# Kernel optimization log

Measured on AMD Instinct MI355X. Metric: run time of the kernel, lower is better.

## Reference

```python
import jax, jax.numpy as jnp
import numpy as np

B, T, ADIM = 64, 2048, 384
NUM_EMB, HID_DIM = 10, 3


def setup_inputs() -> dict:
    key = jax.random.key(0)
    ks = jax.random.split(key, 9)
    return {
        "hs_ref_embs": jax.random.normal(ks[0], (B, T, ADIM), dtype=jnp.float32),
        "inds": jax.random.randint(ks[1], (B, T), 0, NUM_EMB, dtype=jnp.int64),
        "codebook": jax.random.normal(ks[2], (NUM_EMB, HID_DIM), dtype=jnp.float32),
        "W_ih": jax.random.normal(ks[3], (4 * NUM_EMB, ADIM), dtype=jnp.float32) * 0.05,
        "W_hh": jax.random.normal(ks[4], (4 * NUM_EMB, NUM_EMB), dtype=jnp.float32) * 0.05,
        "b_ih": jax.random.normal(ks[5], (4 * NUM_EMB,), dtype=jnp.float32) * 0.05,
        "b_hh": jax.random.normal(ks[6], (4 * NUM_EMB,), dtype=jnp.float32) * 0.05,
        "qs_W": jax.random.normal(ks[7], (ADIM, HID_DIM), dtype=jnp.float32) * 0.05,
        "qs_b": jax.random.normal(ks[8], (ADIM,), dtype=jnp.float32) * 0.05,
    }


def _lstm_cell(x, h, c, W_ih, W_hh, b_ih, b_hh):
    # PyTorch LSTMCell: gates = x @ W_ih^T + b_ih + h @ W_hh^T + b_hh
    gates = x @ W_ih.T + b_ih + h @ W_hh.T + b_hh  # (B, 4H)
    i, f, g, o = jnp.split(gates, 4, axis=-1)
    i, f, o = jax.nn.sigmoid(i), jax.nn.sigmoid(f), jax.nn.sigmoid(o)
    g = jnp.tanh(g)
    c_new = f * c + i * g
    h_new = o * jnp.tanh(c_new)
    return h_new, c_new


def reference(hs_ref_embs, inds, codebook, W_ih, W_hh, b_ih, b_hh, qs_W, qs_b):
    Bsz, Tmax, _ = hs_ref_embs.shape
    H = codebook.shape[0]  # num_embeddings (= LSTM hidden size)
    D = codebook.shape[1]  # hidden_dim

    def step(carry, xs):
        h, c, prev_emb = carry
        x_t, is_first = xs
        qs = prev_emb @ qs_W.T + qs_b  # (B, adim)
        inp = jnp.where(is_first, x_t, x_t + qs)
        h, c = _lstm_cell(inp, h, c, W_ih, W_hh, b_ih, b_hh)
        scores = jax.nn.log_softmax(h, axis=-1)  # (B, H)
        top_ind = jnp.argmax(scores, axis=-1)    # top-1, indices not differentiated
        emb = codebook[top_ind]                  # (B, D) gather == one-hot matmul
        return (h, c, emb), (scores, emb)

    init = (
        jnp.zeros((Bsz, H), hs_ref_embs.dtype),
        jnp.zeros((Bsz, H), hs_ref_embs.dtype),
        jnp.zeros((Bsz, D), hs_ref_embs.dtype),
    )
    xs = (jnp.swapaxes(hs_ref_embs, 0, 1), jnp.arange(Tmax) == 0)
    _, (scores, embs) = jax.lax.scan(step, init, xs)
    scores = jnp.swapaxes(scores, 0, 1)  # (B, T, H) log-probs
    embs = jnp.swapaxes(embs, 0, 1)      # (B, T, D)
    # NLLLoss(mean): -mean over (B,T) of log-prob at ground-truth index
    picked = jnp.take_along_axis(scores, inds[..., None], axis=-1)[..., 0]
    loss = -jnp.mean(picked)
    return embs, loss
```

## Files before the change

kernel.cpp:

```cpp
#include <hip/hip_runtime.h>
#include <math.h>

#define BB 64
#define TT 2048
#define ADIM 384
#define NE 10
#define NG 40
#define HD 3

#define OFF_X64   0ULL
#define OFF_W64T  41943040ULL
#define OFF_ETAB  (OFF_W64T + 122880ULL)
#define OFF_ADD0  (OFF_ETAB + 3200ULL)
#define OFF_ADD1  (OFF_ADD0 + 320ULL)
#define OFF_H     (OFF_ADD1 + 320ULL)
#define OFF_IDX   (OFF_H + 5242880ULL)
#define OFF_PART  (OFF_IDX + 524288ULL)
#define OFF_DUMP  (OFF_PART + 4096ULL)

__device__ __forceinline__ float fexp2(float x) {
    float r;
    asm("v_exp_f32 %0, %1" : "=v"(r) : "v"(x));
    return r;
}
__device__ __forceinline__ float frcp1(float d) {
    float r;
    asm("v_rcp_f32 %0, %1" : "=v"(r) : "v"(d));
    float e = fmaf(-d, r, 1.0f);
    return fmaf(r, e, r);
}

template<int CTRL>
__device__ __forceinline__ float dpp_mov_f32(float x) {
    int v = __float_as_int(x);
    v = __builtin_amdgcn_update_dpp(v, v, CTRL, 0xF, 0xF, true);
    return __int_as_float(v);
}
template<int CTRL, int RMASK>
__device__ __forceinline__ unsigned dpp_mov_u32(unsigned x) {
    int v = __builtin_amdgcn_update_dpp((int)x, (int)x, CTRL, RMASK, 0xF, true);
    return (unsigned)v;
}
__device__ __forceinline__ unsigned umax2(unsigned a, unsigned b) {
    return a > b ? a : b;
}

__global__ __launch_bounds__(256) void setup_kernel(
        const float* __restrict__ W_ih, const float* __restrict__ codebook,
        const float* __restrict__ qs_W, const float* __restrict__ qs_b,
        const float* __restrict__ b_ih, const float* __restrict__ b_hh,
        double* __restrict__ W64T, float* __restrict__ Etab32,
        double* __restrict__ ADD0, double* __restrict__ ADD1) {
    int tid = threadIdx.x;
    if (blockIdx.x == 0) {
        if (tid < NG) {
            int k = tid;
            double M0 = 0, M1 = 0, M2 = 0, qb = 0;
            for (int a = 0; a < ADIM; ++a) {
                double w = (double)W_ih[k * ADIM + a];
                M0 = fma(w, (double)qs_W[a * HD + 0], M0);
                M1 = fma(w, (double)qs_W[a * HD + 1], M1);
                M2 = fma(w, (double)qs_W[a * HD + 2], M2);
                qb = fma(w, (double)qs_b[a], qb);
            }
            for (int i = 0; i < NE; ++i) {
                double e = (double)codebook[i * HD + 0] * M0;
                e = fma((double)codebook[i * HD + 1], M1, e);
                e = fma((double)codebook[i * HD + 2], M2, e);
                Etab32[i * NG + k] = (float)e;
            }
            double bias = (double)b_ih[k] + (double)b_hh[k];
            ADD0[k] = bias;
            ADD1[k] = bias + qb;
        }
    } else {
        int i = (blockIdx.x - 1) * 256 + tid;
        int a = i / NG, kk = i % NG;
        W64T[i] = (double)W_ih[kk * ADIM + a];
    }
}

__global__ __launch_bounds__(256) void gemm_kernel(
        const float* __restrict__ hs, const double* __restrict__ W64T,
        const double* __restrict__ ADD0, const double* __restrict__ ADD1,
        float* __restrict__ X32) {
    int lane = threadIdx.x & 63;
    int wv = threadIdx.x >> 6;
    int cb = __builtin_amdgcn_readfirstlane(wv * 10);
    long row = (long)blockIdx.x * 64 + lane;
    const float* xr = hs + row * ADIM;
    double acc[10];
#pragma unroll
    for (int j = 0; j < 10; ++j) acc[j] = 0.0;
    for (int a0 = 0; a0 < ADIM; a0 += 4) {
        float4 xv = *(const float4*)(xr + a0);
#pragma unroll
        for (int u = 0; u < 4; ++u) {
            double xd = (double)((&xv.x)[u]);
            const double* wp = W64T + (a0 + u) * NG + cb;
#pragma unroll
            for (int j = 0; j < 10; ++j) acc[j] = fma(wp[j], xd, acc[j]);
        }
    }
    int trow = (int)(row & (TT - 1));
    float* op = X32 + row * NG + cb;
#pragma unroll
    for (int j = 0; j < 10; ++j) {
        double a0j = ADD0[cb + j], a1j = ADD1[cb + j];
        op[j] = (float)(acc[j] + (trow == 0 ? a0j : a1j));
    }
}

__global__ __launch_bounds__(64) void recur_kernel(
        const float* __restrict__ X32,
        const float* __restrict__ W_hh, const float* __restrict__ Etab32,
        char* __restrict__ ws) {
    const int k = threadIdx.x;
    const int b = blockIdx.x;
    const int j = k & 3;
    const int m = k >> 2;
    const bool valid = (k < NG);
    const int col = valid ? (j * 10 + m) : (NG - 1);
    const bool isg = (j == 2);

    const float LOG2E = 1.44269504088896340736f;
    const float Lg   = isg ? (-2.0f * LOG2E) : (-LOG2E);
    const float amul = isg ? 2.0f : 1.0f;
    const float aadd = isg ? -1.0f : 0.0f;
    const float L2   = -2.0f * LOG2E;

    float whh[NE];
#pragma unroll
    for (int mm = 0; mm < NE; ++mm) whh[mm] = W_hh[col * NE + mm];
    float etab[NE];
#pragma unroll
    for (int i = 0; i < NE; ++i) etab[i] = Etab32[i * NG + col];

    const float* Xb = X32 + (long)b * TT * NG;

    const bool is_h = ((k & 3) == 0) && valid;
    const bool is_i = (k == NG);
    unsigned voff = is_h ? (unsigned)(OFF_H + ((unsigned)b * TT * NE + m) * 4u)
                  : is_i ? (unsigned)(OFF_IDX + (unsigned)b * TT * 4u)
                         : (unsigned)OFF_DUMP;
    const unsigned vstep = is_h ? (unsigned)(NE * 4) : is_i ? 4u : 0u;

    const unsigned vmask = valid ? 0xFFFFFFFFu : 0u;

    float xs0 = Xb[0 * NG + col];
    float xs1 = Xb[1 * NG + col];
    float xs2 = Xb[2 * NG + col];
    float xs3 = Xb[3 * NG + col];

    float ha[NE];
#pragma unroll
    for (int mm = 0; mm < NE; ++mm) ha[mm] = 0.0f;
    float c = 0.0f, esel = 0.0f;

    auto step = [&](float& xslot, int t) {
        float xg = xslot;
        xslot = Xb[(t + 4) * NG + col];

        float p0 = fmaf(ha[1], whh[1], ha[0] * whh[0]);
        float p1 = fmaf(ha[3], whh[3], ha[2] * whh[2]);
        float p2 = fmaf(ha[5], whh[5], ha[4] * whh[4]);
        float p3 = fmaf(ha[7], whh[7], ha[6] * whh[6]);
        float p4 = fmaf(ha[9], whh[9], ha[8] * whh[8]);
        float dotE = ((p0 + p1) + (p2 + p3)) + (p4 + esel);
        float g32 = xg + dotE;

        float e1 = fexp2(g32 * Lg);
        float r1 = frcp1(1.0f + e1);
        float act = fmaf(amul, r1, aadd);

        float fiv = dpp_mov_f32<0x00>(act);
        float ffv = dpp_mov_f32<0x55>(act);
        float fgv = dpp_mov_f32<0xAA>(act);
        float fov = dpp_mov_f32<0xFF>(act);
        c = fmaf(ffv, c, fiv * fgv);

        float e2 = fexp2(fabsf(c) * L2);
        float r2 = frcp1(1.0f + e2);
        float th = fmaf(2.0f, r2, -1.0f);
        float habs = fov * th;
        int hI = __float_as_int(habs) | (__float_as_int(c) & 0x80000000);

        int smsk = hI >> 31;
        unsigned key0 = ((unsigned)(hI ^ (smsk | (int)0x80000000))) & vmask;
        unsigned kr = umax2(key0, dpp_mov_u32<0x124, 0xF>(key0));
        kr = umax2(kr, dpp_mov_u32<0x128, 0xF>(kr));
        kr = umax2(kr, dpp_mov_u32<0x142, 0xA>(kr));
        kr = umax2(kr, dpp_mov_u32<0x143, 0xC>(kr));
        unsigned sMax = (unsigned)__builtin_amdgcn_readlane((int)kr, 32);
        unsigned long long ball = __ballot(key0 == sMax);
        int s_idx = ((int)__builtin_ctzll(ball)) >> 2;

        int val = is_h ? hI : s_idx;
        *(int*)(ws + voff) = val;
        voff += vstep;

#pragma unroll
        for (int mm = 0; mm < NE; ++mm)
            ha[mm] = __int_as_float(__builtin_amdgcn_readlane(hI, 4 * mm));

        float a0 = (s_idx & 1) ? etab[1] : etab[0];
        float a1 = (s_idx & 1) ? etab[3] : etab[2];
        float a2 = (s_idx & 1) ? etab[5] : etab[4];
        float a3 = (s_idx & 1) ? etab[7] : etab[6];
        float a4 = (s_idx & 1) ? etab[9] : etab[8];
        float b0 = (s_idx & 2) ? a1 : a0;
        float b1 = (s_idx & 2) ? a3 : a2;
        float c0 = (s_idx & 4) ? b1 : b0;
        esel = (s_idx & 8) ? a4 : c0;
    };

    for (int t = 0; t < TT; t += 4) {
        step(xs0, t);
        step(xs1, t + 1);
        step(xs2, t + 2);
        step(xs3, t + 3);
    }
}

__global__ __launch_bounds__(256) void tail_kernel(
        const float* __restrict__ h_ws, const int* __restrict__ idx_ws,
        const int* __restrict__ inds, const float* __restrict__ codebook,
        float* __restrict__ out_embs, double* __restrict__ partials) {
    int i = blockIdx.x * 256 + threadIdx.x;
    int idx = idx_ws[i];
    out_embs[i * 3 + 0] = codebook[idx * 3 + 0];
    out_embs[i * 3 + 1] = codebook[idx * 3 + 1];
    out_embs[i * 3 + 2] = codebook[idx * 3 + 2];

    const float* hp = h_ws + (long)i * NE;
    double hv[NE];
#pragma unroll
    for (int mm = 0; mm < NE; ++mm) hv[mm] = (double)hp[mm];
    double mx = hv[0];
#pragma unroll
    for (int mm = 1; mm < NE; ++mm) mx = fmax(mx, hv[mm]);
    double sdn = 0.0;
#pragma unroll
    for (int mm = 0; mm < NE; ++mm) sdn += exp(hv[mm] - mx);
    int ind = inds[i];
    double picked = (double)hp[ind] - (mx + log(sdn));

    __shared__ double red[256];
    red[threadIdx.x] = picked;
    __syncthreads();
    for (int st = 128; st > 0; st >>= 1) {
        if (threadIdx.x < st) red[threadIdx.x] += red[threadIdx.x + st];
        __syncthreads();
    }
    if (threadIdx.x == 0) partials[blockIdx.x] = red[0];
}

__global__ __launch_bounds__(256) void final_kernel(
        const double* __restrict__ partials, float* __restrict__ out_loss) {
    __shared__ double red[256];
    red[threadIdx.x] = partials[threadIdx.x] + partials[threadIdx.x + 256];
    __syncthreads();
    for (int st = 128; st > 0; st >>= 1) {
        if (threadIdx.x < st) red[threadIdx.x] += red[threadIdx.x + st];
        __syncthreads();
    }
    if (threadIdx.x == 0)
        out_loss[0] = (float)(-red[0] / (double)(BB * TT));
}

extern "C" void kernel_launch(void* const* d_in, const int* in_sizes, int n_in,
                              void* d_out, int out_size, void* d_ws, size_t ws_size,
                              hipStream_t stream) {
    const float* hs       = (const float*)d_in[0];
    const int*   inds     = (const int*)d_in[1];
    const float* codebook = (const float*)d_in[2];
    const float* W_ih     = (const float*)d_in[3];
    const float* W_hh     = (const float*)d_in[4];
    const float* b_ih     = (const float*)d_in[5];
    const float* b_hh     = (const float*)d_in[6];
    const float* qs_W     = (const float*)d_in[7];
    const float* qs_b     = (const float*)d_in[8];
    float* out = (float*)d_out;

    char* ws = (char*)d_ws;
    float*  X32   = (float*)(ws + OFF_X64);
    double* W64T  = (double*)(ws + OFF_W64T);
    float*  Etab32= (float*)(ws + OFF_ETAB);
    double* ADD0  = (double*)(ws + OFF_ADD0);
    double* ADD1  = (double*)(ws + OFF_ADD1);
    float*  h_ws  = (float*)(ws + OFF_H);
    int*    idx_ws= (int*)(ws + OFF_IDX);
    double* part  = (double*)(ws + OFF_PART);

    setup_kernel<<<61, 256, 0, stream>>>(W_ih, codebook, qs_W, qs_b, b_ih, b_hh,
                                         W64T, Etab32, ADD0, ADD1);
    gemm_kernel<<<2048, 256, 0, stream>>>(hs, W64T, ADD0, ADD1, X32);
    recur_kernel<<<BB, 64, 0, stream>>>(X32, W_hh, Etab32, ws);
    tail_kernel<<<512, 256, 0, stream>>>(h_ws, idx_ws, inds, codebook, out, part);
    final_kernel<<<1, 256, 0, stream>>>(part, out + (size_t)BB * TT * HD);
}
```

Baseline: 595.4 us.

## Switch input GEMM to fp32, fold biases into embedding table, drop rcp refinement

The input projection GEMM now runs in fp32 directly on W_ih rows with split accumulators, replacing the fp64 path that needed a pre-transposed double weight copy. The per-step bias, including the query-side bias, is folded into the embedding gate table, and the first step's bias is seeded separately. The Newton refinement after v_rcp_f32 is removed in the recurrence. This cuts fp64 GEMM cost and per-step latency, at the risk of argmax flips from the lower precision.

```diff
diff --git a/kernel.cpp b/kernel.cpp
--- a/kernel.cpp
+++ b/kernel.cpp
@@ -8,12 +8,10 @@
 #define NG 40
 #define HD 3
 
-#define OFF_X64   0ULL
-#define OFF_W64T  41943040ULL
-#define OFF_ETAB  (OFF_W64T + 122880ULL)
-#define OFF_ADD0  (OFF_ETAB + 3200ULL)
-#define OFF_ADD1  (OFF_ADD0 + 320ULL)
-#define OFF_H     (OFF_ADD1 + 320ULL)
+#define OFF_X32   0ULL
+#define OFF_ETAB  (41943040ULL + 122880ULL)
+#define OFF_BIAS0 (OFF_ETAB + 3200ULL)
+#define OFF_H     (OFF_BIAS0 + 320ULL)
 #define OFF_IDX   (OFF_H + 5242880ULL)
 #define OFF_PART  (OFF_IDX + 524288ULL)
 #define OFF_DUMP  (OFF_PART + 4096ULL)
@@ -23,11 +21,10 @@
     asm("v_exp_f32 %0, %1" : "=v"(r) : "v"(x));
     return r;
 }
-__device__ __forceinline__ float frcp1(float d) {
+__device__ __forceinline__ float frcp(float d) {
     float r;
     asm("v_rcp_f32 %0, %1" : "=v"(r) : "v"(d));
-    float e = fmaf(-d, r, 1.0f);
-    return fmaf(r, e, r);
+    return r;
 }
 
 template<int CTRL>
@@ -45,76 +42,63 @@
     return a > b ? a : b;
 }
 
-__global__ __launch_bounds__(256) void setup_kernel(
+__global__ __launch_bounds__(64) void setup_kernel(
         const float* __restrict__ W_ih, const float* __restrict__ codebook,
         const float* __restrict__ qs_W, const float* __restrict__ qs_b,
         const float* __restrict__ b_ih, const float* __restrict__ b_hh,
-        double* __restrict__ W64T, float* __restrict__ Etab32,
-        double* __restrict__ ADD0, double* __restrict__ ADD1) {
-    int tid = threadIdx.x;
-    if (blockIdx.x == 0) {
-        if (tid < NG) {
-            int k = tid;
-            double M0 = 0, M1 = 0, M2 = 0, qb = 0;
-            for (int a = 0; a < ADIM; ++a) {
-                double w = (double)W_ih[k * ADIM + a];
-                M0 = fma(w, (double)qs_W[a * HD + 0], M0);
-                M1 = fma(w, (double)qs_W[a * HD + 1], M1);
-                M2 = fma(w, (double)qs_W[a * HD + 2], M2);
-                qb = fma(w, (double)qs_b[a], qb);
-            }
-            for (int i = 0; i < NE; ++i) {
-                double e = (double)codebook[i * HD + 0] * M0;
-                e = fma((double)codebook[i * HD + 1], M1, e);
-                e = fma((double)codebook[i * HD + 2], M2, e);
-                Etab32[i * NG + k] = (float)e;
-            }
-            double bias = (double)b_ih[k] + (double)b_hh[k];
-            ADD0[k] = bias;
-            ADD1[k] = bias + qb;
-        }
-    } else {
-        int i = (blockIdx.x - 1) * 256 + tid;
-        int a = i / NG, kk = i % NG;
-        W64T[i] = (double)W_ih[kk * ADIM + a];
-    }
+        float* __restrict__ EtabB, float* __restrict__ BIAS0) {
+    int k = threadIdx.x;
+    if (k >= NG) return;
+    double M0 = 0, M1 = 0, M2 = 0, qb = 0;
+    for (int a = 0; a < ADIM; ++a) {
+        double w = (double)W_ih[k * ADIM + a];
+        M0 = fma(w, (double)qs_W[a * HD + 0], M0);
+        M1 = fma(w, (double)qs_W[a * HD + 1], M1);
+        M2 = fma(w, (double)qs_W[a * HD + 2], M2);
+        qb = fma(w, (double)qs_b[a], qb);
+    }
+    double bias = (double)b_ih[k] + (double)b_hh[k];
+    for (int i = 0; i < NE; ++i) {
+        double e = bias + qb;
+        e = fma((double)codebook[i * HD + 0], M0, e);
+        e = fma((double)codebook[i * HD + 1], M1, e);
+        e = fma((double)codebook[i * HD + 2], M2, e);
+        EtabB[i * NG + k] = (float)e;
+    }
+    BIAS0[k] = (float)bias;
 }
 
 __global__ __launch_bounds__(256) void gemm_kernel(
-        const float* __restrict__ hs, const double* __restrict__ W64T,
-        const double* __restrict__ ADD0, const double* __restrict__ ADD1,
+        const float* __restrict__ hs, const float* __restrict__ W_ih,
         float* __restrict__ X32) {
     int lane = threadIdx.x & 63;
     int wv = threadIdx.x >> 6;
     int cb = __builtin_amdgcn_readfirstlane(wv * 10);
     long row = (long)blockIdx.x * 64 + lane;
     const float* xr = hs + row * ADIM;
-    double acc[10];
-#pragma unroll
-    for (int j = 0; j < 10; ++j) acc[j] = 0.0;
+    float accA[10], accB[10];
+#pragma unroll
+    for (int j = 0; j < 10; ++j) { accA[j] = 0.0f; accB[j] = 0.0f; }
     for (int a0 = 0; a0 < ADIM; a0 += 4) {
         float4 xv = *(const float4*)(xr + a0);
 #pragma unroll
-        for (int u = 0; u < 4; ++u) {
-            double xd = (double)((&xv.x)[u]);
-            const double* wp = W64T + (a0 + u) * NG + cb;
-#pragma unroll
-            for (int j = 0; j < 10; ++j) acc[j] = fma(wp[j], xd, acc[j]);
+        for (int j = 0; j < 10; ++j) {
+            float4 wv4 = *(const float4*)(W_ih + (cb + j) * ADIM + a0);
+            accA[j] = fmaf(wv4.x, xv.x, accA[j]);
+            accA[j] = fmaf(wv4.y, xv.y, accA[j]);
+            accB[j] = fmaf(wv4.z, xv.z, accB[j]);
+            accB[j] = fmaf(wv4.w, xv.w, accB[j]);
         }
     }
-    int trow = (int)(row & (TT - 1));
     float* op = X32 + row * NG + cb;
 #pragma unroll
-    for (int j = 0; j < 10; ++j) {
-        double a0j = ADD0[cb + j], a1j = ADD1[cb + j];
-        op[j] = (float)(acc[j] + (trow == 0 ? a0j : a1j));
-    }
+    for (int j = 0; j < 10; ++j) op[j] = accA[j] + accB[j];
 }
 
 __global__ __launch_bounds__(64) void recur_kernel(
         const float* __restrict__ X32,
-        const float* __restrict__ W_hh, const float* __restrict__ Etab32,
-        char* __restrict__ ws) {
+        const float* __restrict__ W_hh, const float* __restrict__ EtabB,
+        const float* __restrict__ BIAS0, char* __restrict__ ws) {
     const int k = threadIdx.x;
     const int b = blockIdx.x;
     const int j = k & 3;
@@ -134,7 +118,7 @@
     for (int mm = 0; mm < NE; ++mm) whh[mm] = W_hh[col * NE + mm];
     float etab[NE];
 #pragma unroll
-    for (int i = 0; i < NE; ++i) etab[i] = Etab32[i * NG + col];
+    for (int i = 0; i < NE; ++i) etab[i] = EtabB[i * NG + col];
 
     const float* Xb = X32 + (long)b * TT * NG;
 
@@ -155,7 +139,8 @@
     float ha[NE];
 #pragma unroll
     for (int mm = 0; mm < NE; ++mm) ha[mm] = 0.0f;
-    float c = 0.0f, esel = 0.0f;
+    float c = 0.0f;
+    float esel = BIAS0[col];
 
     auto step = [&](float& xslot, int t) {
         float xg = xslot;
@@ -170,7 +155,7 @@
         float g32 = xg + dotE;
 
         float e1 = fexp2(g32 * Lg);
-        float r1 = frcp1(1.0f + e1);
+        float r1 = frcp(1.0f + e1);
         float act = fmaf(amul, r1, aadd);
 
         float fiv = dpp_mov_f32<0x00>(act);
@@ -180,7 +165,7 @@
         c = fmaf(ffv, c, fiv * fgv);
 
         float e2 = fexp2(fabsf(c) * L2);
-        float r2 = frcp1(1.0f + e2);
+        float r2 = frcp(1.0f + e2);
         float th = fmaf(2.0f, r2, -1.0f);
         float habs = fov * th;
         int hI = __float_as_int(habs) | (__float_as_int(c) & 0x80000000);
@@ -283,19 +268,17 @@
     float* out = (float*)d_out;
 
     char* ws = (char*)d_ws;
-    float*  X32   = (float*)(ws + OFF_X64);
-    double* W64T  = (double*)(ws + OFF_W64T);
-    float*  Etab32= (float*)(ws + OFF_ETAB);
-    double* ADD0  = (double*)(ws + OFF_ADD0);
-    double* ADD1  = (double*)(ws + OFF_ADD1);
+    float*  X32   = (float*)(ws + OFF_X32);
+    float*  EtabB = (float*)(ws + OFF_ETAB);
+    float*  BIAS0 = (float*)(ws + OFF_BIAS0);
     float*  h_ws  = (float*)(ws + OFF_H);
     int*    idx_ws= (int*)(ws + OFF_IDX);
     double* part  = (double*)(ws + OFF_PART);
 
-    setup_kernel<<<61, 256, 0, stream>>>(W_ih, codebook, qs_W, qs_b, b_ih, b_hh,
-                                         W64T, Etab32, ADD0, ADD1);
-    gemm_kernel<<<2048, 256, 0, stream>>>(hs, W64T, ADD0, ADD1, X32);
-    recur_kernel<<<BB, 64, 0, stream>>>(X32, W_hh, Etab32, ws);
+    setup_kernel<<<1, 64, 0, stream>>>(W_ih, codebook, qs_W, qs_b, b_ih, b_hh,
+                                       EtabB, BIAS0);
+    gemm_kernel<<<2048, 256, 0, stream>>>(hs, W_ih, X32);
+    recur_kernel<<<BB, 64, 0, stream>>>(X32, W_hh, EtabB, BIAS0, ws);
     tail_kernel<<<512, 256, 0, stream>>>(h_ws, idx_ws, inds, codebook, out, part);
     final_kernel<<<1, 256, 0, stream>>>(part, out + (size_t)BB * TT * HD);
 }
```

New measurement: 570.2 us. 4.2% less time.
